# Performance work log

Hardware: AMD Instinct MI355X
Metric: run time of the kernel (lower is better)

Reference implementation:

```python
import jax, jax.numpy as jnp
import numpy as np

G, N, E = 16, 512, 2048        # graphs, nodes/graph, edges/graph
CN, CE = 64, 64                # node / edge feature channels
K = 3                          # Laguerre polynomial order
RATIO = 0.5
KEEP = int(np.ceil(RATIO * N)) # 256 kept nodes per graph (static)
POWER_ITERS = 64               # power iteration approximating eigsh(k=1,'LM')


def setup_inputs() -> dict:
    key = jax.random.key(0)
    ks = jax.random.split(key, 10)
    x_n = jax.random.normal(ks[0], (G * N, CN), jnp.float32)
    x_e = jax.random.normal(ks[1], (G * E, CE), jnp.float32)
    # incidence endpoints per edge, local node ids, no self loops
    u = jax.random.randint(ks[2], (G, E), 0, N)
    v = (u + 1 + jax.random.randint(ks[3], (G, E), 0, N - 1)) % N
    # node-level conv graph (global ids within per-graph blocks): both directions
    offs = (jnp.arange(G) * N)[:, None]
    src_n = jnp.concatenate([(u + offs).reshape(-1), (v + offs).reshape(-1)])
    dst_n = jnp.concatenate([(v + offs).reshape(-1), (u + offs).reshape(-1)])
    edge_weight_n = jax.random.uniform(ks[4], (src_n.shape[0],), jnp.float32)
    # edge-level conv graph (global ids within per-graph edge blocks)
    ME = 4 * E
    offs_e = (jnp.arange(G) * E)[:, None]
    src_e = (jax.random.randint(ks[5], (G, ME), 0, E) + offs_e).reshape(-1)
    dst_e = (jax.random.randint(ks[6], (G, ME), 0, E) + offs_e).reshape(-1)
    edge_weight_e = jax.random.uniform(ks[7], (src_e.shape[0],), jnp.float32)
    # HodgeLaguerreConv(C -> 1, K) weights (glorot-ish) + bias (zeros init)
    W_n = jax.random.normal(ks[8], (K, CN), jnp.float32) / np.sqrt(CN)
    b_n = jnp.zeros((1,), jnp.float32)
    W_e = jax.random.normal(ks[9], (K, CE), jnp.float32) / np.sqrt(CE)
    b_e = jnp.zeros((1,), jnp.float32)
    return dict(x_n=x_n, x_e=x_e, edge_u=u, edge_v=v,
                src_n=src_n, dst_n=dst_n, edge_weight_n=edge_weight_n,
                src_e=src_e, dst_e=dst_e, edge_weight_e=edge_weight_e,
                W_n=W_n, b_n=b_n, W_e=W_e, b_e=b_e)


def hodge_laguerre(x, src, dst, w, Wk, b):
    """HodgeLaguerreConv with out_channels=1: out = sum_k T_k(L) x @ Wk[k] + b.
    T_0 = x; T_1 = x - Lx; T_{k+1} = (-L T_k + (2k+1) T_k - k T_{k-1})/(k+1)."""
    num = x.shape[0]
    def L(z):  # scatter-add message passing: out[i] = sum_{j->i} norm * z[j]
        return jax.ops.segment_sum(w[:, None] * z[src], dst, num_segments=num)
    Tx0 = x
    out = Tx0 @ Wk[0]
    Tx1 = x - L(x)
    out = out + Tx1 @ Wk[1]
    k = 1
    for i in range(2, Wk.shape[0]):
        Tx2 = (-L(Tx1) + (2 * k + 1) * Tx1 - k * Tx0) / (k + 1)
        out = out + Tx2 @ Wk[i]
        Tx0, Tx1 = Tx1, Tx2
        k += 1
    return out + b[0]


def pool_graph(sn, se, xn, xe, u, v):
    # node score augmented by |B1| @ edge_score (abs incidence gathers both endpoints)
    aug = sn.at[u].add(se).at[v].add(se)
    perm = jnp.argsort(-aug)                    # descending sort, take top KEEP
    mask_n = jnp.zeros((N,), xn.dtype).at[perm[:KEEP]].set(1.0)
    # mask_e = |B1|^T (1 - mask_n); keep edge iff both endpoints kept (== 0)
    bad = (1.0 - mask_n[u]) + (1.0 - mask_n[v])
    keep_e = (bad == 0.0).astype(xn.dtype)
    # dense incidence B1 [N, E]: -1 at source row, +1 at target row
    cols = jnp.arange(E)
    B = jnp.zeros((N, E), xn.dtype).at[u, cols].add(-1.0).at[v, cols].add(1.0)
    Bm = B * mask_n[:, None] * keep_e[None, :]  # row/col masking (zero-padded)
    L0 = Bm @ Bm.T                              # [N, N] node Laplacian
    L1 = Bm.T @ Bm                              # [E, E] edge Laplacian
    # power iteration for lambda_max(L0) (== eigsh k=1 'LM'; zero rows keep spectrum)
    w = jnp.ones((N,), xn.dtype) / np.sqrt(N)
    for _ in range(POWER_ITERS):
        w = L0 @ w
        w = w / (jnp.linalg.norm(w) + 1e-12)
    lam = w @ (L0 @ w)
    scale = 2.0 / (lam + 1e-12)
    return xn * mask_n[:, None], L0 * scale, xe * keep_e[:, None], L1 * scale


def reference(x_n, x_e, edge_u, edge_v, src_n, dst_n, edge_weight_n,
              src_e, dst_e, edge_weight_e, W_n, b_n, W_e, b_e):
    score_n = jax.nn.sigmoid(hodge_laguerre(x_n, src_n, dst_n, edge_weight_n, W_n, b_n).reshape(-1))
    score_e = jax.nn.sigmoid(hodge_laguerre(x_e, src_e, dst_e, edge_weight_e, W_e, b_e).reshape(-1))
    xn_g = (x_n * score_n[:, None]).reshape(G, N, CN)
    xe_g = (x_e * score_e[:, None]).reshape(G, E, CE)
    sn = score_n.reshape(G, N)
    se = score_e.reshape(G, E)
    return jax.vmap(pool_graph)(sn, se, xn_g, xe_g, edge_u, edge_v)
```

## Files before the change

### kernel.cpp

```cpp
#include <hip/hip_runtime.h>
#include <math.h>

#define GG 16
#define NNODE 512
#define EEDGE 2048
#define KEEPN 256
#define PITERS 64
#define NNT 8192
#define NET 32768

typedef float vfloat4 __attribute__((ext_vector_type(4)));

#define WS_C1N 0
#define WS_C2N 8192
#define WS_BN  16384
#define WS_C1E 24576
#define WS_C2E 57344
#define WS_BE  90112
#define WS_SNW 122880
#define WS_SEW 131072
#define WS_KLIST 163840
#define WS_KCNT 196608
#define WS_SCALE 196624

#define O_XN 0
#define O_L0 524288
#define O_XE 4718592
#define O_L1 6815744

#define L04 1048576
#define ZTOT4 17825792

#define DCAP 12

__global__ __launch_bounds__(512) void k_front(
    const float* __restrict__ xn, const float* __restrict__ xe,
    const float* __restrict__ Wn, const float* __restrict__ We,
    float* __restrict__ ws, float* __restrict__ out) {
  const int tid = threadIdx.x, bid = blockIdx.x;
  if (bid >= 1024) {
    vfloat4 z = (vfloat4)(0.f);
    vfloat4* o4 = (vfloat4*)out;
    int base = (bid - 1024) * 512 + tid;
    #pragma unroll
    for (int n = 0; n < 17; ++n) {
      int i = base + n * 1048576;
      int f = (i < L04) ? (O_L0 / 4 + i) : (O_L1 / 4 + (i - L04));
      __builtin_nontemporal_store(z, &o4[f]);
    }
    return;
  }
  const int lane = tid & 63;
  const int wv = (bid * 512 + tid) >> 6;
  #pragma unroll
  for (int n = 0; n < 5; ++n) {
    int gw = wv + n * 8192;
    const float* x; const float* W; int row; float *c1, *c2, *bs;
    if (gw < NNT) {
      row = gw; x = xn + (size_t)row * 64; W = Wn;
      c1 = ws + WS_C1N; c2 = ws + WS_C2N; bs = ws + WS_BN;
    } else {
      row = gw - NNT;
      x = xe + (size_t)row * 64; W = We;
      c1 = ws + WS_C1E; c2 = ws + WS_C2E; bs = ws + WS_BE;
    }
    float v = x[lane];
    float r0 = v * W[lane];
    float r1 = v * W[64 + lane];
    float r2 = v * W[128 + lane];
    for (int o = 32; o; o >>= 1) {
      r0 += __shfl_xor(r0, o, 64);
      r1 += __shfl_xor(r1, o, 64);
      r2 += __shfl_xor(r2, o, 64);
    }
    if (lane == 0) { c1[row] = r1; c2[row] = r2; bs[row] = r0 + r1 + r2; }
  }
}

#define SM_AUG 0
#define SM_SNW 512
#define SM_RED 1024
#define SM_IWS 1032
#define SM_KCP 1040
#define SM_S0  1056
#define SM_TOT 9256
__global__ __launch_bounds__(512) void k_pipe(
    const int* __restrict__ src_n, const int* __restrict__ dst_n, const float* __restrict__ wn,
    const int* __restrict__ src_e, const int* __restrict__ dst_e, const float* __restrict__ we,
    const int* __restrict__ edge_u, const int* __restrict__ edge_v,
    const float* __restrict__ bnp, const float* __restrict__ bep,
    float* __restrict__ ws) {
  const int tid = threadIdx.x;
  __shared__ float smem[SM_TOT];
  int* smi = (int*)smem;
  float* aug = smem + SM_AUG;
  float* snw = smem + SM_SNW;
  float* red = smem + SM_RED;
  int*   iws = smi + SM_IWS;
  int*   kcp = smi + SM_KCP;

  const int g = blockIdx.x;
  const int roffN = g * NNODE;
  const int roffE = g * EEDGE;
  const int lane = tid & 63, wid = tid >> 6;
  float biasN = bnp[0], biasE = bep[0];

  {
    float* c1n = smem + SM_S0;
    float* c2n = smem + SM_S0 + 512;
    float* d1n = smem + SM_S0 + 1024;
    float* d2n = smem + SM_S0 + 1536;
    float* e2n = smem + SM_S0 + 2048;
    c1n[tid] = ws[WS_C1N + roffN + tid];
    c2n[tid] = ws[WS_C2N + roffN + tid];
    d1n[tid] = 0.f; d2n[tid] = 0.f; e2n[tid] = 0.f;
    __syncthreads();
    for (int t = tid; t < 4096; t += 512) {
      int idx = (t < 2048) ? (g * 2048 + t) : (32768 + g * 2048 + (t - 2048));
      int s = src_n[idx] - roffN, d = dst_n[idx] - roffN;
      float w = wn[idx];
      atomicAdd(&d1n[d], w * c1n[s]);
      atomicAdd(&d2n[d], w * c2n[s]);
    }
    __syncthreads();
    for (int t = tid; t < 4096; t += 512) {
      int idx = (t < 2048) ? (g * 2048 + t) : (32768 + g * 2048 + (t - 2048));
      int s = src_n[idx] - roffN, d = dst_n[idx] - roffN;
      atomicAdd(&e2n[d], wn[idx] * d2n[s]);
    }
    __syncthreads();
    float t = ws[WS_BN + roffN + tid] - d1n[tid] - 2.0f * d2n[tid]
            + 0.5f * e2n[tid] + biasN;
    float s = 1.0f / (1.0f + expf(-t));
    snw[tid] = s; aug[tid] = s;
    __syncthreads();
  }

  float* seS = smem + SM_S0 + 2048;
  int*   suv = smi + SM_S0;
  {
    float* c1e = smem + SM_S0;
    float* c2e = smem + SM_S0 + 2048;
    float* d1e = smem + SM_S0 + 4096;
    float* d2e = smem + SM_S0 + 6144;
    float* e2e = smem + SM_S0;
    for (int i = tid; i < EEDGE; i += 512) {
      c1e[i] = ws[WS_C1E + roffE + i];
      c2e[i] = ws[WS_C2E + roffE + i];
      d1e[i] = 0.f; d2e[i] = 0.f;
    }
    __syncthreads();
    for (int t = tid; t < 8192; t += 512) {
      int idx = g * 8192 + t;
      int s = src_e[idx] - roffE, d = dst_e[idx] - roffE;
      float w = we[idx];
      atomicAdd(&d1e[d], w * c1e[s]);
      atomicAdd(&d2e[d], w * c2e[s]);
    }
    __syncthreads();
    for (int i = tid; i < EEDGE; i += 512) e2e[i] = 0.f;
    __syncthreads();
    for (int t = tid; t < 8192; t += 512) {
      int idx = g * 8192 + t;
      int s = src_e[idx] - roffE, d = dst_e[idx] - roffE;
      atomicAdd(&e2e[d], we[idx] * d2e[s]);
    }
    __syncthreads();
    for (int e = tid; e < EEDGE; e += 512) {
      float t = ws[WS_BE + roffE + e] - d1e[e] - 2.0f * d2e[e]
              + 0.5f * e2e[e] + biasE;
      float s = 1.0f / (1.0f + expf(-t));
      int u = edge_u[roffE + e], v = edge_v[roffE + e];
      seS[e] = s;
      suv[e] = u | (v << 16);
      atomicAdd(&aug[u], s);
      atomicAdd(&aug[v], s);
    }
    __syncthreads();
  }

  unsigned short* adjU = (unsigned short*)(smem + SM_S0 + 4096);
  float* wvA = smem + SM_S0 + 6144;
  float* wvB = smem + SM_S0 + 6660;
  int* maskS = smi + SM_S0 + 7176;
  int* degS  = smi + SM_S0 + 7688;
  int* offS  = smi + SM_SNW;

  {
    float a = aug[tid];
    int r = 0;
    #pragma unroll 8
    for (int j = 0; j < NNODE; ++j) {
      float b = aug[j];
      r += (b > a) || (b == a && j < tid);
    }
    maskS[tid] = (r < KEEPN) ? 1 : 0;
    degS[tid] = 0;
  }
  if (tid == 0) *kcp = 0;
  __syncthreads();
  ws[WS_SNW + roffN + tid] = snw[tid] * (float)maskS[tid];

  int* wsi = (int*)ws;
  for (int e = tid; e < EEDGE; e += 512) {
    int p2 = suv[e];
    int u = p2 & 0xffff, v = p2 >> 16;
    int k = maskS[u] & maskS[v];
    ws[WS_SEW + roffE + e] = seS[e] * (float)k;
    if (k) {
      int p = atomicAdd(kcp, 1);
      wsi[WS_KLIST + roffE + p] = e;
      atomicAdd(&degS[u], 1);
      atomicAdd(&degS[v], 1);
    }
  }
  __syncthreads();
  if (tid == 0) wsi[WS_KCNT + g] = *kcp;

  int dv = degS[tid];
  int inc = dv;
  for (int o = 1; o < 64; o <<= 1) {
    int t = __shfl_up(inc, o, 64);
    if (lane >= o) inc += t;
  }
  if (lane == 63) iws[wid] = inc;
  __syncthreads();
  int base = 0;
  for (int k = 0; k < wid; ++k) base += iws[k];
  int myStart = base + inc - dv;
  offS[tid] = myStart;
  __syncthreads();

  for (int e = tid; e < EEDGE; e += 512) {
    int p2 = suv[e];
    int u = p2 & 0xffff, v = p2 >> 16;
    if (maskS[u] & maskS[v]) {
      int pu = atomicAdd(&offS[u], 1); adjU[pu] = (unsigned short)v;
      int pv = atomicAdd(&offS[v], 1); adjU[pv] = (unsigned short)u;
    }
  }
  __syncthreads();
  int myDeg = dv;
  int myEnd = myStart + myDeg;

  int nbr[DCAP];
  #pragma unroll
  for (int k = 0; k < DCAP; ++k)
    nbr[k] = (k < myDeg) ? (int)adjU[myStart + k] : NNODE;
  bool ovf = myDeg > DCAP;

  wvA[tid] = 0.04419417382415922f;
  if (tid == 0) { wvA[NNODE] = 0.f; wvB[NNODE] = 0.f; }
  __syncthreads();
  float* wcur = wvA; float* wnext = wvB;
  for (int it = 0; it < PITERS; ++it) {
    float acc = (float)myDeg * wcur[tid];
    #pragma unroll
    for (int k = 0; k < DCAP; ++k) acc -= wcur[nbr[k]];
    if (ovf) for (int p = myStart + DCAP; p < myEnd; ++p) acc -= wcur[(int)adjU[p]];
    if ((it & 7) == 7) {
      float sq = acc * acc;
      for (int o = 32; o; o >>= 1) sq += __shfl_xor(sq, o, 64);
      if (lane == 0) red[wid] = sq;
      __syncthreads();
      float tot = red[0] + red[1] + red[2] + red[3]
                + red[4] + red[5] + red[6] + red[7];
      wnext[tid] = acc * (1.0f / (sqrtf(tot) + 1e-12f));
    } else {
      wnext[tid] = acc;
    }
    __syncthreads();
    float* tmp = wcur; wcur = wnext; wnext = tmp;
  }
  {
    float wv_ = wcur[tid];
    float acc = (float)myDeg * wv_;
    #pragma unroll
    for (int k = 0; k < DCAP; ++k) acc -= wcur[nbr[k]];
    if (ovf) for (int p = myStart + DCAP; p < myEnd; ++p) acc -= wcur[(int)adjU[p]];
    float pr = wv_ * acc;
    for (int o = 32; o; o >>= 1) pr += __shfl_xor(pr, o, 64);
    if (lane == 0) red[wid] = pr;
    __syncthreads();
    if (tid == 0) {
      float lam = red[0] + red[1] + red[2] + red[3]
                + red[4] + red[5] + red[6] + red[7];
      ws[WS_SCALE + g] = 2.0f / (lam + 1e-12f);
    }
  }
}

__global__ __launch_bounds__(256) void k_out(
    const float* __restrict__ xn, const float* __restrict__ xe,
    const int* __restrict__ edge_u, const int* __restrict__ edge_v,
    const float* __restrict__ ws, float* __restrict__ out) {
  int b = blockIdx.x, tid = threadIdx.x;
  const int* wsi = (const int*)ws;
  if (b < 512) {
    int idx = b * 256 + tid;
    int row = idx >> 4;
    float s = ws[WS_SNW + row];
    float4 x4 = ((const float4*)xn)[idx];
    ((float4*)(out + O_XN))[idx] = make_float4(x4.x * s, x4.y * s, x4.z * s, x4.w * s);
  } else if (b < 2560) {
    int idx = (b - 512) * 256 + tid;
    int row = idx >> 4;
    float s = ws[WS_SEW + row];
    float4 x4 = ((const float4*)xe)[idx];
    ((float4*)(out + O_XE))[idx] = make_float4(x4.x * s, x4.y * s, x4.z * s, x4.w * s);
  } else if (b < 2576) {
    int g = b - 2560;
    int cnt = wsi[WS_KCNT + g];
    float s = ws[WS_SCALE + g];
    float* L0 = out + O_L0 + (long long)g * (NNODE * NNODE);
    const int* kl = wsi + WS_KLIST + g * EEDGE;
    const int* eu = edge_u + g * EEDGE;
    const int* ev = edge_v + g * EEDGE;
    for (int t = tid; t < cnt; t += 256) {
      int e = kl[t];
      int u = eu[e], v = ev[e];
      atomicAdd(&L0[u * NNODE + u], s);
      atomicAdd(&L0[v * NNODE + v], s);
      atomicAdd(&L0[u * NNODE + v], -s);
      atomicAdd(&L0[v * NNODE + u], -s);
    }
  } else {
    int q = b - 2576;
    int g = q >> 8, sb = q & 255;
    int cnt = wsi[WS_KCNT + g];
    float s = ws[WS_SCALE + g];
    float* L1 = out + O_L1 + (long long)g * (EEDGE * EEDGE);
    const int* kl = wsi + WS_KLIST + g * EEDGE;
    const int* eu = edge_u + g * EEDGE;
    const int* ev = edge_v + g * EEDGE;
    for (int a = sb; a < cnt; a += 256) {
      int e1 = kl[a];
      int u1 = eu[e1], v1 = ev[e1];
      long long rowoff = (long long)e1 * EEDGE;
      for (int b2 = tid; b2 < cnt; b2 += 256) {
        int e2 = kl[b2];
        int u2 = eu[e2], v2 = ev[e2];
        int val = (u1 == u2) + (v1 == v2) - (v1 == u2) - (u1 == v2);
        if (val) L1[rowoff + e2] = s * (float)val;
      }
    }
  }
}

extern "C" void kernel_launch(void* const* d_in, const int* in_sizes, int n_in,
                              void* d_out, int out_size, void* d_ws, size_t ws_size,
                              hipStream_t stream) {
  const float* x_n = (const float*)d_in[0];
  const float* x_e = (const float*)d_in[1];
  const int* edge_u = (const int*)d_in[2];
  const int* edge_v = (const int*)d_in[3];
  const int* src_n = (const int*)d_in[4];
  const int* dst_n = (const int*)d_in[5];
  const float* ew_n = (const float*)d_in[6];
  const int* src_e = (const int*)d_in[7];
  const int* dst_e = (const int*)d_in[8];
  const float* ew_e = (const float*)d_in[9];
  const float* W_n = (const float*)d_in[10];
  const float* b_n = (const float*)d_in[11];
  const float* W_e = (const float*)d_in[12];
  const float* b_e = (const float*)d_in[13];
  float* ws = (float*)d_ws;
  float* out = (float*)d_out;

  k_front<<<3072, 512, 0, stream>>>(x_n, x_e, W_n, W_e, ws, out);
  k_pipe<<<16, 512, 0, stream>>>(src_n, dst_n, ew_n, src_e, dst_e, ew_e,
                                 edge_u, edge_v, b_n, b_e, ws);
  k_out<<<6672, 256, 0, stream>>>(x_n, x_e, edge_u, edge_v, ws, out);
}
```

Before: 489.0 us.

## Overlap output zero-fill with serial graph pipeline and prefetch edge indices

The bulk zero-fill of the L0/L1 output regions moves from the front dot-product kernel into extra blocks of the 16-block pipeline kernel. Those blocks run alongside the per-graph serial work and use otherwise idle CUs. The scatter loops in the pipeline kernel are also software-pipelined: each iteration loads the next edge's src/dst/weight before issuing the current LDS atomics, to hide global load latency. The risk is that the zero-fill blocks contend for memory bandwidth with the graph blocks or delay their scheduling.

```diff
diff --git a/kernel.cpp b/kernel.cpp
--- a/kernel.cpp
+++ b/kernel.cpp
@@ -33,23 +33,11 @@
 
 #define DCAP 12
 
-__global__ __launch_bounds__(512) void k_front(
+__global__ __launch_bounds__(512) void k_dots(
     const float* __restrict__ xn, const float* __restrict__ xe,
     const float* __restrict__ Wn, const float* __restrict__ We,
-    float* __restrict__ ws, float* __restrict__ out) {
+    float* __restrict__ ws) {
   const int tid = threadIdx.x, bid = blockIdx.x;
-  if (bid >= 1024) {
-    vfloat4 z = (vfloat4)(0.f);
-    vfloat4* o4 = (vfloat4*)out;
-    int base = (bid - 1024) * 512 + tid;
-    #pragma unroll
-    for (int n = 0; n < 17; ++n) {
-      int i = base + n * 1048576;
-      int f = (i < L04) ? (O_L0 / 4 + i) : (O_L1 / 4 + (i - L04));
-      __builtin_nontemporal_store(z, &o4[f]);
-    }
-    return;
-  }
   const int lane = tid & 63;
   const int wv = (bid * 512 + tid) >> 6;
   #pragma unroll
@@ -89,8 +77,20 @@
     const int* __restrict__ src_e, const int* __restrict__ dst_e, const float* __restrict__ we,
     const int* __restrict__ edge_u, const int* __restrict__ edge_v,
     const float* __restrict__ bnp, const float* __restrict__ bep,
-    float* __restrict__ ws) {
+    float* __restrict__ ws, float* __restrict__ out) {
   const int tid = threadIdx.x;
+  if (blockIdx.x >= 16) {
+    vfloat4 z = (vfloat4)(0.f);
+    vfloat4* o4 = (vfloat4*)out;
+    int base = (blockIdx.x - 16) * 512 + tid;
+    #pragma unroll
+    for (int n = 0; n < 17; ++n) {
+      int i = base + n * 1048576;
+      int f = (i < L04) ? (O_L0 / 4 + i) : (O_L1 / 4 + (i - L04));
+      __builtin_nontemporal_store(z, &o4[f]);
+    }
+    return;
+  }
   __shared__ float smem[SM_TOT];
   int* smi = (int*)smem;
   float* aug = smem + SM_AUG;
@@ -115,18 +115,37 @@
     c2n[tid] = ws[WS_C2N + roffN + tid];
     d1n[tid] = 0.f; d2n[tid] = 0.f; e2n[tid] = 0.f;
     __syncthreads();
-    for (int t = tid; t < 4096; t += 512) {
-      int idx = (t < 2048) ? (g * 2048 + t) : (32768 + g * 2048 + (t - 2048));
-      int s = src_n[idx] - roffN, d = dst_n[idx] - roffN;
-      float w = wn[idx];
-      atomicAdd(&d1n[d], w * c1n[s]);
-      atomicAdd(&d2n[d], w * c2n[s]);
-    }
-    __syncthreads();
-    for (int t = tid; t < 4096; t += 512) {
-      int idx = (t < 2048) ? (g * 2048 + t) : (32768 + g * 2048 + (t - 2048));
-      int s = src_n[idx] - roffN, d = dst_n[idx] - roffN;
-      atomicAdd(&e2n[d], wn[idx] * d2n[s]);
+    {
+      int t = tid;
+      int idx = g * 2048 + t;
+      int s = src_n[idx], d = dst_n[idx]; float w = wn[idx];
+      while (t < 4096) {
+        int tn = t + 512;
+        int sN = 0, dN = roffN; float wN = 0.f;
+        if (tn < 4096) {
+          int idxN = (tn < 2048) ? (g * 2048 + tn) : (32768 + g * 2048 + (tn - 2048));
+          sN = src_n[idxN]; dN = dst_n[idxN]; wN = wn[idxN];
+        }
+        atomicAdd(&d1n[d - roffN], w * c1n[s - roffN]);
+        atomicAdd(&d2n[d - roffN], w * c2n[s - roffN]);
+        t = tn; s = sN; d = dN; w = wN;
+      }
+    }
+    __syncthreads();
+    {
+      int t = tid;
+      int idx = g * 2048 + t;
+      int s = src_n[idx], d = dst_n[idx]; float w = wn[idx];
+      while (t < 4096) {
+        int tn = t + 512;
+        int sN = 0, dN = roffN; float wN = 0.f;
+        if (tn < 4096) {
+          int idxN = (tn < 2048) ? (g * 2048 + tn) : (32768 + g * 2048 + (tn - 2048));
+          sN = src_n[idxN]; dN = dst_n[idxN]; wN = wn[idxN];
+        }
+        atomicAdd(&e2n[d - roffN], w * d2n[s - roffN]);
+        t = tn; s = sN; d = dN; w = wN;
+      }
     }
     __syncthreads();
     float t = ws[WS_BN + roffN + tid] - d1n[tid] - 2.0f * d2n[tid]
@@ -150,20 +169,39 @@
       d1e[i] = 0.f; d2e[i] = 0.f;
     }
     __syncthreads();
-    for (int t = tid; t < 8192; t += 512) {
+    {
+      int t = tid;
       int idx = g * 8192 + t;
-      int s = src_e[idx] - roffE, d = dst_e[idx] - roffE;
-      float w = we[idx];
-      atomicAdd(&d1e[d], w * c1e[s]);
-      atomicAdd(&d2e[d], w * c2e[s]);
+      int s = src_e[idx], d = dst_e[idx]; float w = we[idx];
+      while (t < 8192) {
+        int tn = t + 512;
+        int sN = 0, dN = roffE; float wN = 0.f;
+        if (tn < 8192) {
+          int idxN = g * 8192 + tn;
+          sN = src_e[idxN]; dN = dst_e[idxN]; wN = we[idxN];
+        }
+        atomicAdd(&d1e[d - roffE], w * c1e[s - roffE]);
+        atomicAdd(&d2e[d - roffE], w * c2e[s - roffE]);
+        t = tn; s = sN; d = dN; w = wN;
+      }
     }
     __syncthreads();
     for (int i = tid; i < EEDGE; i += 512) e2e[i] = 0.f;
     __syncthreads();
-    for (int t = tid; t < 8192; t += 512) {
+    {
+      int t = tid;
       int idx = g * 8192 + t;
-      int s = src_e[idx] - roffE, d = dst_e[idx] - roffE;
-      atomicAdd(&e2e[d], we[idx] * d2e[s]);
+      int s = src_e[idx], d = dst_e[idx]; float w = we[idx];
+      while (t < 8192) {
+        int tn = t + 512;
+        int sN = 0, dN = roffE; float wN = 0.f;
+        if (tn < 8192) {
+          int idxN = g * 8192 + tn;
+          sN = src_e[idxN]; dN = dst_e[idxN]; wN = we[idxN];
+        }
+        atomicAdd(&e2e[d - roffE], w * d2e[s - roffE]);
+        t = tn; s = sN; d = dN; w = wN;
+      }
     }
     __syncthreads();
     for (int e = tid; e < EEDGE; e += 512) {
@@ -367,8 +405,8 @@
   float* ws = (float*)d_ws;
   float* out = (float*)d_out;
 
-  k_front<<<3072, 512, 0, stream>>>(x_n, x_e, W_n, W_e, ws, out);
-  k_pipe<<<16, 512, 0, stream>>>(src_n, dst_n, ew_n, src_e, dst_e, ew_e,
-                                 edge_u, edge_v, b_n, b_e, ws);
+  k_dots<<<1024, 512, 0, stream>>>(x_n, x_e, W_n, W_e, ws);
+  k_pipe<<<16 + 2048, 512, 0, stream>>>(src_n, dst_n, ew_n, src_e, dst_e, ew_e,
+                                        edge_u, edge_v, b_n, b_e, ws, out);
   k_out<<<6672, 256, 0, stream>>>(x_n, x_e, edge_u, edge_v, ws, out);
 }
```

Result: faster. 467.3 us (-4.4%).

## Overlap output zero-fill with per-graph pipeline and batch edge loads before atomics

Applied to the files above, without the earlier changes.

Moves the large zero-fill of the L0/L1 output regions out of the front dot-product kernel and into extra blocks of the 16-block pipeline kernel, so the fill runs on otherwise idle CUs while the serial per-graph work executes. Inside the pipeline kernel, edge indices and weights are loaded into registers up front and reused across both scatter passes, and the float4 staging loads are vectorised. In the power-iteration loop the neighbour gathers are hoisted into a register array so the loads can be issued together. This raises register pressure, and the fill blocks compete with the pipeline blocks for memory bandwidth and scheduling.

```diff
diff --git a/kernel.cpp b/kernel.cpp
--- a/kernel.cpp
+++ b/kernel.cpp
@@ -33,23 +33,11 @@
 
 #define DCAP 12
 
-__global__ __launch_bounds__(512) void k_front(
+__global__ __launch_bounds__(512) void k_dots(
     const float* __restrict__ xn, const float* __restrict__ xe,
     const float* __restrict__ Wn, const float* __restrict__ We,
-    float* __restrict__ ws, float* __restrict__ out) {
+    float* __restrict__ ws) {
   const int tid = threadIdx.x, bid = blockIdx.x;
-  if (bid >= 1024) {
-    vfloat4 z = (vfloat4)(0.f);
-    vfloat4* o4 = (vfloat4*)out;
-    int base = (bid - 1024) * 512 + tid;
-    #pragma unroll
-    for (int n = 0; n < 17; ++n) {
-      int i = base + n * 1048576;
-      int f = (i < L04) ? (O_L0 / 4 + i) : (O_L1 / 4 + (i - L04));
-      __builtin_nontemporal_store(z, &o4[f]);
-    }
-    return;
-  }
   const int lane = tid & 63;
   const int wv = (bid * 512 + tid) >> 6;
   #pragma unroll
@@ -84,13 +72,25 @@
 #define SM_KCP 1040
 #define SM_S0  1056
 #define SM_TOT 9256
-__global__ __launch_bounds__(512) void k_pipe(
+__global__ __launch_bounds__(512, 2) void k_pipe(
     const int* __restrict__ src_n, const int* __restrict__ dst_n, const float* __restrict__ wn,
     const int* __restrict__ src_e, const int* __restrict__ dst_e, const float* __restrict__ we,
     const int* __restrict__ edge_u, const int* __restrict__ edge_v,
     const float* __restrict__ bnp, const float* __restrict__ bep,
-    float* __restrict__ ws) {
+    float* __restrict__ ws, float* __restrict__ out) {
   const int tid = threadIdx.x;
+  if (blockIdx.x >= 16) {
+    vfloat4 z = (vfloat4)(0.f);
+    vfloat4* o4 = (vfloat4*)out;
+    int base = (blockIdx.x - 16) * 512 + tid;
+    #pragma unroll
+    for (int n = 0; n < 17; ++n) {
+      int i = base + n * 1048576;
+      int f = (i < L04) ? (O_L0 / 4 + i) : (O_L1 / 4 + (i - L04));
+      __builtin_nontemporal_store(z, &o4[f]);
+    }
+    return;
+  }
   __shared__ float smem[SM_TOT];
   int* smi = (int*)smem;
   float* aug = smem + SM_AUG;
@@ -114,20 +114,23 @@
     c1n[tid] = ws[WS_C1N + roffN + tid];
     c2n[tid] = ws[WS_C2N + roffN + tid];
     d1n[tid] = 0.f; d2n[tid] = 0.f; e2n[tid] = 0.f;
-    __syncthreads();
-    for (int t = tid; t < 4096; t += 512) {
-      int idx = (t < 2048) ? (g * 2048 + t) : (32768 + g * 2048 + (t - 2048));
-      int s = src_n[idx] - roffN, d = dst_n[idx] - roffN;
-      float w = wn[idx];
-      atomicAdd(&d1n[d], w * c1n[s]);
-      atomicAdd(&d2n[d], w * c2n[s]);
-    }
-    __syncthreads();
-    for (int t = tid; t < 4096; t += 512) {
-      int idx = (t < 2048) ? (g * 2048 + t) : (32768 + g * 2048 + (t - 2048));
-      int s = src_n[idx] - roffN, d = dst_n[idx] - roffN;
-      atomicAdd(&e2n[d], wn[idx] * d2n[s]);
-    }
+    int sN[8], dN[8]; float wN[8];
+    #pragma unroll
+    for (int n = 0; n < 8; ++n) {
+      int t = tid + n * 512;
+      int idx = (n < 4) ? (g * 2048 + t) : (32768 + g * 2048 + (t - 2048));
+      sN[n] = src_n[idx] - roffN; dN[n] = dst_n[idx] - roffN; wN[n] = wn[idx];
+    }
+    __syncthreads();
+    #pragma unroll
+    for (int n = 0; n < 8; ++n) {
+      atomicAdd(&d1n[dN[n]], wN[n] * c1n[sN[n]]);
+      atomicAdd(&d2n[dN[n]], wN[n] * c2n[sN[n]]);
+    }
+    __syncthreads();
+    #pragma unroll
+    for (int n = 0; n < 8; ++n)
+      atomicAdd(&e2n[dN[n]], wN[n] * d2n[sN[n]]);
     __syncthreads();
     float t = ws[WS_BN + roffN + tid] - d1n[tid] - 2.0f * d2n[tid]
             + 0.5f * e2n[tid] + biasN;
@@ -144,37 +147,50 @@
     float* d1e = smem + SM_S0 + 4096;
     float* d2e = smem + SM_S0 + 6144;
     float* e2e = smem + SM_S0;
-    for (int i = tid; i < EEDGE; i += 512) {
-      c1e[i] = ws[WS_C1E + roffE + i];
-      c2e[i] = ws[WS_C2E + roffE + i];
-      d1e[i] = 0.f; d2e[i] = 0.f;
-    }
-    __syncthreads();
-    for (int t = tid; t < 8192; t += 512) {
-      int idx = g * 8192 + t;
-      int s = src_e[idx] - roffE, d = dst_e[idx] - roffE;
-      float w = we[idx];
-      atomicAdd(&d1e[d], w * c1e[s]);
-      atomicAdd(&d2e[d], w * c2e[s]);
-    }
-    __syncthreads();
-    for (int i = tid; i < EEDGE; i += 512) e2e[i] = 0.f;
-    __syncthreads();
-    for (int t = tid; t < 8192; t += 512) {
-      int idx = g * 8192 + t;
-      int s = src_e[idx] - roffE, d = dst_e[idx] - roffE;
-      atomicAdd(&e2e[d], we[idx] * d2e[s]);
-    }
-    __syncthreads();
-    for (int e = tid; e < EEDGE; e += 512) {
-      float t = ws[WS_BE + roffE + e] - d1e[e] - 2.0f * d2e[e]
-              + 0.5f * e2e[e] + biasE;
+    {
+      float4 a = ((const float4*)(ws + WS_C1E + roffE))[tid];
+      float4 b = ((const float4*)(ws + WS_C2E + roffE))[tid];
+      ((float4*)c1e)[tid] = a;
+      ((float4*)c2e)[tid] = b;
+      ((float4*)d1e)[tid] = make_float4(0.f, 0.f, 0.f, 0.f);
+      ((float4*)d2e)[tid] = make_float4(0.f, 0.f, 0.f, 0.f);
+    }
+    int sE[16], dE[16]; float wE[16];
+    #pragma unroll
+    for (int n = 0; n < 16; ++n) {
+      int idx = g * 8192 + n * 512 + tid;
+      sE[n] = src_e[idx] - roffE; dE[n] = dst_e[idx] - roffE; wE[n] = we[idx];
+    }
+    __syncthreads();
+    #pragma unroll
+    for (int n = 0; n < 16; ++n) {
+      atomicAdd(&d1e[dE[n]], wE[n] * c1e[sE[n]]);
+      atomicAdd(&d2e[dE[n]], wE[n] * c2e[sE[n]]);
+    }
+    __syncthreads();
+    ((float4*)e2e)[tid] = make_float4(0.f, 0.f, 0.f, 0.f);
+    __syncthreads();
+    #pragma unroll
+    for (int n = 0; n < 16; ++n)
+      atomicAdd(&e2e[dE[n]], wE[n] * d2e[sE[n]]);
+    float bR[4]; int uR[4], vR[4];
+    #pragma unroll
+    for (int n = 0; n < 4; ++n) {
+      int e = tid + n * 512;
+      bR[n] = ws[WS_BE + roffE + e];
+      uR[n] = edge_u[roffE + e];
+      vR[n] = edge_v[roffE + e];
+    }
+    __syncthreads();
+    #pragma unroll
+    for (int n = 0; n < 4; ++n) {
+      int e = tid + n * 512;
+      float t = bR[n] - d1e[e] - 2.0f * d2e[e] + 0.5f * e2e[e] + biasE;
       float s = 1.0f / (1.0f + expf(-t));
-      int u = edge_u[roffE + e], v = edge_v[roffE + e];
       seS[e] = s;
-      suv[e] = u | (v << 16);
-      atomicAdd(&aug[u], s);
-      atomicAdd(&aug[v], s);
+      suv[e] = uR[n] | (vR[n] << 16);
+      atomicAdd(&aug[uR[n]], s);
+      atomicAdd(&aug[vR[n]], s);
     }
     __syncthreads();
   }
@@ -254,9 +270,12 @@
   __syncthreads();
   float* wcur = wvA; float* wnext = wvB;
   for (int it = 0; it < PITERS; ++it) {
+    float tg[DCAP];
+    #pragma unroll
+    for (int k = 0; k < DCAP; ++k) tg[k] = wcur[nbr[k]];
     float acc = (float)myDeg * wcur[tid];
     #pragma unroll
-    for (int k = 0; k < DCAP; ++k) acc -= wcur[nbr[k]];
+    for (int k = 0; k < DCAP; ++k) acc -= tg[k];
     if (ovf) for (int p = myStart + DCAP; p < myEnd; ++p) acc -= wcur[(int)adjU[p]];
     if ((it & 7) == 7) {
       float sq = acc * acc;
@@ -273,10 +292,13 @@
     float* tmp = wcur; wcur = wnext; wnext = tmp;
   }
   {
+    float tg[DCAP];
+    #pragma unroll
+    for (int k = 0; k < DCAP; ++k) tg[k] = wcur[nbr[k]];
     float wv_ = wcur[tid];
     float acc = (float)myDeg * wv_;
     #pragma unroll
-    for (int k = 0; k < DCAP; ++k) acc -= wcur[nbr[k]];
+    for (int k = 0; k < DCAP; ++k) acc -= tg[k];
     if (ovf) for (int p = myStart + DCAP; p < myEnd; ++p) acc -= wcur[(int)adjU[p]];
     float pr = wv_ * acc;
     for (int o = 32; o; o >>= 1) pr += __shfl_xor(pr, o, 64);
@@ -367,8 +389,8 @@
   float* ws = (float*)d_ws;
   float* out = (float*)d_out;
 
-  k_front<<<3072, 512, 0, stream>>>(x_n, x_e, W_n, W_e, ws, out);
-  k_pipe<<<16, 512, 0, stream>>>(src_n, dst_n, ew_n, src_e, dst_e, ew_e,
-                                 edge_u, edge_v, b_n, b_e, ws);
+  k_dots<<<1024, 512, 0, stream>>>(x_n, x_e, W_n, W_e, ws);
+  k_pipe<<<16 + 2048, 512, 0, stream>>>(src_n, dst_n, ew_n, src_e, dst_e, ew_e,
+                                        edge_u, edge_v, b_n, b_e, ws, out);
   k_out<<<6672, 256, 0, stream>>>(x_n, x_e, edge_u, edge_v, ws, out);
 }
```

Result: faster. 455.2 us (-6.9%).
